# Kernel optimization log

Hardware: AMD Instinct MI355X
Metric: run time of the kernel (lower is better)

Reference implementation:

```python
import jax, jax.numpy as jnp
import numpy as np

WIN = 8          # window size (8x8), hardcoded in SelfAttention
DIM_HEAD = 32    # hardcoded dim_head
LN_EPS = 1e-5


def _rel_pos_index():
    # Reproduces the buffer computed in SelfAttention.__init__ (torch.meshgrid default = 'ij')
    coords = np.stack(np.meshgrid(np.arange(WIN), np.arange(WIN), indexing='ij'))  # (2,8,8)
    flat = coords.reshape(2, -1)                      # (2,64)
    rel = flat[:, :, None] - flat[:, None, :]         # (2,64,64)
    rel = rel.transpose(1, 2, 0).copy()               # (64,64,2)
    rel[:, :, 0] += WIN - 1
    rel[:, :, 1] += WIN - 1
    rel[:, :, 0] *= 2 * WIN - 1
    return jnp.asarray(rel.sum(-1))                   # (64,64) int32, values in [0,225)

REL_IDX = _rel_pos_index()


def setup_inputs() -> dict:
    key = jax.random.key(0)
    ks = jax.random.split(key, 8)
    B, H, W, C = 16, 64, 64, 512
    nh = C // DIM_HEAD
    N = WIN * WIN
    nwin = B * (H // WIN) * (W // WIN)   # 1024 windows total
    inner = 4 * C                        # MLP(expansion_ratio=4, gated=False)
    s = 0.02
    return {
        'x': jax.random.normal(ks[0], (B, H, W, C), jnp.float32),
        'q': jax.random.normal(ks[1], (nwin, N, C), jnp.float32),
        'k': jax.random.normal(ks[2], (nwin, N, C), jnp.float32),
        'v': jax.random.normal(ks[3], (nwin, N, C), jnp.float32),
        'proj_w': jax.random.normal(ks[4], (C, C), jnp.float32) * s,
        'proj_b': jnp.zeros((C,), jnp.float32),
        'rpb_table': jax.random.normal(ks[5], ((2 * WIN - 1) ** 2, nh), jnp.float32) * s,
        'gamma1': jnp.full((C,), 1e-5, jnp.float32),   # LayerScale init_values
        'ln2_w': jnp.ones((C,), jnp.float32),
        'ln2_b': jnp.zeros((C,), jnp.float32),
        'fc1_w': jax.random.normal(ks[6], (inner, C), jnp.float32) * s,
        'fc1_b': jnp.zeros((inner,), jnp.float32),
        'fc2_w': jax.random.normal(ks[7], (C, inner), jnp.float32) * s,
        'fc2_b': jnp.zeros((C,), jnp.float32),
        'gamma2': jnp.full((C,), 1e-5, jnp.float32),
    }


def _layernorm(x, w, b):
    mu = x.mean(-1, keepdims=True)
    var = ((x - mu) ** 2).mean(-1, keepdims=True)
    return (x - mu) * jax.lax.rsqrt(var + LN_EPS) * w + b


def _block(x, q, k, v, proj_w, proj_b, rpb_table, gamma1, ln2_w, ln2_b,
           fc1_w, fc1_b, fc2_w, fc2_b, gamma2):
    B, H, W, C = x.shape
    nh = C // DIM_HEAD
    N = WIN * WIN
    scale = DIM_HEAD ** -0.5
    BW = q.shape[0]  # B * num_windows
    # heads: (BW, nh, N, dh)
    qh = q.reshape(BW, N, nh, DIM_HEAD).transpose(0, 2, 1, 3)
    kh = k.reshape(BW, N, nh, DIM_HEAD).transpose(0, 2, 1, 3)
    vh = v.reshape(BW, N, nh, DIM_HEAD).transpose(0, 2, 1, 3)
    attn = jnp.einsum('bhnd,bhmd->bhnm', qh, kh) * scale
    attn = jax.nn.softmax(attn, axis=-1)
    # NOTE: faithful to source — relative-position bias is added AFTER softmax.
    bias = rpb_table[REL_IDX].transpose(2, 0, 1)  # (nh, 64, 64)
    attn = attn + bias[None]
    out = jnp.einsum('bhnm,bhmd->bhnd', attn, vh)
    out = out.transpose(0, 2, 1, 3).reshape(BW, N, C)
    out = out @ proj_w.T + proj_b
    # window_reverse -> (B, H, W, C)
    attn_out = out.reshape(B, H // WIN, W // WIN, WIN, WIN, C)
    attn_out = attn_out.transpose(0, 1, 3, 2, 4, 5).reshape(B, H, W, C)
    x = x + gamma1 * attn_out                      # LayerScale residual
    h = _layernorm(x, ln2_w, ln2_b)
    h = jax.nn.gelu(h @ fc1_w.T + fc1_b, approximate=False) @ fc2_w.T + fc2_b
    return x + gamma2 * h


def reference(x, q, k, v, proj_w, proj_b, rpb_table, gamma1, ln2_w, ln2_b,
              fc1_w, fc1_b, fc2_w, fc2_b, gamma2):
    return _block(x, q, k, v, proj_w, proj_b, rpb_table, gamma1, ln2_w, ln2_b,
                  fc1_w, fc1_b, fc2_w, fc2_b, gamma2)
```

## Files before the change

kernel.cpp:

```cpp
#include <hip/hip_runtime.h>
#include <math.h>

typedef __attribute__((ext_vector_type(4))) float f32x4;
typedef __attribute__((ext_vector_type(8))) short bf16x8;
typedef __attribute__((ext_vector_type(4))) unsigned short u16x4;
typedef __attribute__((ext_vector_type(8))) unsigned short u16x8;

__device__ __forceinline__ unsigned short f2bf(float f) {
  union { float f; unsigned u; } v; v.f = f;
  return (unsigned short)((v.u + 0x7fffu + ((v.u >> 16) & 1u)) >> 16);
}

__device__ __forceinline__ f32x4 zero4() {
  f32x4 z; z[0] = z[1] = z[2] = z[3] = 0.f; return z;
}

__device__ __forceinline__ f32x4 mfma16(bf16x8 a, bf16x8 b, f32x4 c) {
  return __builtin_amdgcn_mfma_f32_16x16x32_bf16(a, b, c, 0, 0, 0);
}

__device__ __forceinline__ void gload_lds16(const void* g, void* l) {
  __builtin_amdgcn_global_load_lds(
      (const __attribute__((address_space(1))) unsigned int*)g,
      (__attribute__((address_space(3))) unsigned int*)l, 16, 0, 0);
}

__global__ void cvt_kernel(const float* __restrict__ pw, const float* __restrict__ f1,
                           const float* __restrict__ f2, const float* __restrict__ lnw,
                           const float* __restrict__ lnb, const float* __restrict__ f1b,
                           unsigned short* __restrict__ opw, unsigned short* __restrict__ ow1,
                           unsigned short* __restrict__ of2, float* __restrict__ of1bp) {
  const long stride = (long)gridDim.x * blockDim.x;
  const long t0 = (long)blockIdx.x * blockDim.x + threadIdx.x;
  for (long i = t0; i < 512L * 512; i += stride) opw[i] = f2bf(pw[i]);
  for (long i = t0; i < 2048L * 512; i += stride)
    ow1[i] = f2bf(f1[i] * lnw[i & 511]);
  for (long i = t0; i < 512L * 2048; i += stride) of2[i] = f2bf(f2[i]);
  for (long i = t0; i < 2048; i += stride) {
    float s = f1b[i];
    const float* fr = f1 + i * 512;
    for (int c = 0; c < 512; ++c) s += fr[c] * lnb[c];
    of1bp[i] = s;
  }
}

__global__ __launch_bounds__(256) void attn_kernel(
    const float* __restrict__ q, const float* __restrict__ k,
    const float* __restrict__ v, const float* __restrict__ rpb,
    unsigned short* __restrict__ O) {
  __shared__ __align__(16) unsigned short Plds[4][64][72];
  const int w = blockIdx.x;
  const int tid = threadIdx.x;
  const int wv = tid >> 6;
  const int lane = tid & 63;
  const int l16 = lane & 15;
  const int g = lane >> 4;
  unsigned short (*P)[72] = Plds[wv];
  const float scale = 0.17677669529663687f;
  const long base = (long)w * (64 * 512);

  for (int hi = 0; hi < 4; ++hi) {
    const int h = wv * 4 + hi;
    bf16x8 aq[4], bk[4];
#pragma unroll
    for (int t = 0; t < 4; ++t) {
      const float* qp = q + base + (long)(t * 16 + l16) * 512 + h * 32 + g * 8;
      const float* kp = k + base + (long)(t * 16 + l16) * 512 + h * 32 + g * 8;
      f32x4 q0 = *(const f32x4*)qp, q1 = *(const f32x4*)(qp + 4);
      f32x4 k0 = *(const f32x4*)kp, k1 = *(const f32x4*)(kp + 4);
#pragma unroll
      for (int j = 0; j < 4; ++j) {
        aq[t][j]     = (short)f2bf(q0[j] * scale);
        aq[t][j + 4] = (short)f2bf(q1[j] * scale);
        bk[t][j]     = (short)f2bf(k0[j]);
        bk[t][j + 4] = (short)f2bf(k1[j]);
      }
    }
    f32x4 acc[4][4];
#pragma unroll
    for (int a = 0; a < 4; ++a)
#pragma unroll
      for (int b = 0; b < 4; ++b) acc[a][b] = zero4();
#pragma unroll
    for (int a = 0; a < 4; ++a)
#pragma unroll
      for (int b = 0; b < 4; ++b) acc[a][b] = mfma16(aq[a], bk[b], acc[a][b]);

#pragma unroll
    for (int tm = 0; tm < 4; ++tm) {
      f32x4 mx;
#pragma unroll
      for (int i = 0; i < 4; ++i)
        mx[i] = fmaxf(fmaxf(acc[tm][0][i], acc[tm][1][i]),
                      fmaxf(acc[tm][2][i], acc[tm][3][i]));
#pragma unroll
      for (int off = 1; off < 16; off <<= 1)
#pragma unroll
        for (int i = 0; i < 4; ++i)
          mx[i] = fmaxf(mx[i], __shfl_xor(mx[i], off, 64));
      f32x4 sm = zero4();
#pragma unroll
      for (int tc = 0; tc < 4; ++tc)
#pragma unroll
        for (int i = 0; i < 4; ++i) {
          acc[tm][tc][i] = __expf(acc[tm][tc][i] - mx[i]);
          sm[i] += acc[tm][tc][i];
        }
#pragma unroll
      for (int off = 1; off < 16; off <<= 1)
#pragma unroll
        for (int i = 0; i < 4; ++i) sm[i] += __shfl_xor(sm[i], off, 64);
      f32x4 inv;
#pragma unroll
      for (int i = 0; i < 4; ++i) inv[i] = 1.0f / sm[i];
#pragma unroll
      for (int tc = 0; tc < 4; ++tc)
#pragma unroll
        for (int i = 0; i < 4; ++i) {
          int n = tm * 16 + g * 4 + i;
          int m = tc * 16 + l16;
          int idx = ((n >> 3) - (m >> 3) + 7) * 15 + ((n & 7) - (m & 7) + 7);
          P[n][m] = f2bf(acc[tm][tc][i] * inv[i] + rpb[idx * 16 + h]);
        }
    }

    f32x4 oc[4][2];
#pragma unroll
    for (int a = 0; a < 4; ++a) { oc[a][0] = zero4(); oc[a][1] = zero4(); }
#pragma unroll
    for (int ks = 0; ks < 2; ++ks) {
      bf16x8 ap[4];
#pragma unroll
      for (int tm = 0; tm < 4; ++tm)
        ap[tm] = *(const bf16x8*)&P[tm * 16 + l16][ks * 32 + g * 8];
      bf16x8 bv[2];
#pragma unroll
      for (int tn = 0; tn < 2; ++tn)
#pragma unroll
        for (int j = 0; j < 8; ++j) {
          int m = ks * 32 + g * 8 + j;
          bv[tn][j] = (short)f2bf(v[base + (long)m * 512 + h * 32 + tn * 16 + l16]);
        }
#pragma unroll
      for (int tm = 0; tm < 4; ++tm)
#pragma unroll
        for (int tn = 0; tn < 2; ++tn) oc[tm][tn] = mfma16(ap[tm], bv[tn], oc[tm][tn]);
    }
#pragma unroll
    for (int tm = 0; tm < 4; ++tm)
#pragma unroll
      for (int tn = 0; tn < 2; ++tn)
#pragma unroll
        for (int i = 0; i < 4; ++i) {
          int n = tm * 16 + g * 4 + i;
          O[base + (long)n * 512 + h * 32 + tn * 16 + l16] = f2bf(oc[tm][tn][i]);
        }
  }
}

__global__ __launch_bounds__(256) void proj_kernel(
    const unsigned short* __restrict__ O, const unsigned short* __restrict__ pw,
    const float* __restrict__ pb, const float* __restrict__ gamma1,
    const float* __restrict__ x, float* __restrict__ y) {
  const int w = blockIdx.x;
  const int tid = threadIdx.x;
  const int wv = tid >> 6, lane = tid & 63;
  const int l16 = lane & 15, g = lane >> 4;
  const long obase = (long)w * (64 * 512);
  f32x4 acc[4][8];
#pragma unroll
  for (int a = 0; a < 4; ++a)
#pragma unroll
    for (int b = 0; b < 8; ++b) acc[a][b] = zero4();

  for (int kk = 0; kk < 512; kk += 32) {
    bf16x8 a[4];
#pragma unroll
    for (int tm = 0; tm < 4; ++tm)
      a[tm] = *(const bf16x8*)(O + obase + (long)(tm * 16 + l16) * 512 + kk + g * 8);
#pragma unroll
    for (int tn = 0; tn < 8; ++tn) {
      int c = wv * 128 + tn * 16 + l16;
      bf16x8 b = *(const bf16x8*)(pw + (long)c * 512 + kk + g * 8);
#pragma unroll
      for (int tm = 0; tm < 4; ++tm) acc[tm][tn] = mfma16(a[tm], b, acc[tm][tn]);
    }
  }
  const int bi = w >> 6, wh = (w >> 3) & 7, wc = w & 7;
#pragma unroll
  for (int tn = 0; tn < 8; ++tn) {
    int c = wv * 128 + tn * 16 + l16;
    float g1c = gamma1[c], pbc = pb[c];
#pragma unroll
    for (int tm = 0; tm < 4; ++tm)
#pragma unroll
      for (int i = 0; i < 4; ++i) {
        int n = tm * 16 + g * 4 + i;
        long t = (long)(bi * 64 + wh * 8 + (n >> 3)) * 64 + wc * 8 + (n & 7);
        y[t * 512 + c] = x[t * 512 + c] + g1c * (acc[tm][tn][i] + pbc);
      }
  }
}

__global__ __launch_bounds__(256) void ln_stats_kernel(const float* __restrict__ y,
                                                       float* __restrict__ murs) {
  const int tid = threadIdx.x;
  const long row = (long)blockIdx.x * 64 + (tid >> 2);
  const int sg = tid & 3;
  const float* yr = y + row * 512 + sg * 128;
  float s = 0.f, s2 = 0.f;
  for (int j = 0; j < 128; j += 4) {
    f32x4 t = *(const f32x4*)(yr + j);
    s += t[0] + t[1] + t[2] + t[3];
    s2 += t[0] * t[0] + t[1] * t[1] + t[2] * t[2] + t[3] * t[3];
  }
  s += __shfl_xor(s, 1, 64);  s += __shfl_xor(s, 2, 64);
  s2 += __shfl_xor(s2, 1, 64); s2 += __shfl_xor(s2, 2, 64);
  if (sg == 0) {
    float mu = s * (1.f / 512.f);
    murs[row * 2] = mu;
    murs[row * 2 + 1] = rsqrtf(s2 * (1.f / 512.f) - mu * mu + 1e-5f);
  }
}

__global__ __launch_bounds__(256, 3) void fc1_kernel(
    const float* __restrict__ y, const float* __restrict__ murs,
    const unsigned short* __restrict__ w1s, const float* __restrict__ f1bp,
    unsigned short* __restrict__ h1, int tok0) {
  __shared__ __align__(16) unsigned char smem[17408];
  unsigned short* As = (unsigned short*)smem;
  unsigned short* Bs = (unsigned short*)(smem + 8192);
  unsigned short* ep = (unsigned short*)smem;
  const int bid = blockIdx.x;
  const int ct = bid & 15, rt = bid >> 4;
  const int c0 = ct * 128;
  const int tid = threadIdx.x;
  const int wv = tid >> 6, lane = tid & 63;
  const int l16 = lane & 15, g = lane >> 4;
  const int wr = wv >> 1, wc = wv & 1;
  const long t0 = (long)tok0 + (long)rt * 128;

  const int sr = tid >> 1, sh = tid & 1;
  const float mu = murs[(t0 + sr) * 2];
  const float rs = murs[(t0 + sr) * 2 + 1];
  const float* xr = y + (t0 + sr) * 512 + sh * 16;

  f32x4 acc[4][4];
#pragma unroll
  for (int a = 0; a < 4; ++a)
#pragma unroll
    for (int b = 0; b < 4; ++b) acc[a][b] = zero4();

  for (int kk = 0; kk < 512; kk += 32) {
    f32x4 xv[4];
#pragma unroll
    for (int j = 0; j < 4; ++j) xv[j] = *(const f32x4*)(xr + kk + j * 4);
    u16x8 p0, p1;
#pragma unroll
    for (int e = 0; e < 4; ++e) {
      p0[e]     = f2bf((xv[0][e] - mu) * rs);
      p0[e + 4] = f2bf((xv[1][e] - mu) * rs);
      p1[e]     = f2bf((xv[2][e] - mu) * rs);
      p1[e + 4] = f2bf((xv[3][e] - mu) * rs);
    }
    *(u16x8*)(As + sr * 32 + sh * 16) = p0;
    *(u16x8*)(As + sr * 32 + sh * 16 + 8) = p1;
#pragma unroll
    for (int iss = 0; iss < 2; ++iss) {
      int r = wv * 32 + iss * 16 + (lane >> 2);
      gload_lds16(w1s + (long)(c0 + r) * 512 + kk + (lane & 3) * 8,
                  Bs + (wv * 32 + iss * 16) * 32);
    }
    __syncthreads();
    bf16x8 a[4], b[4];
#pragma unroll
    for (int tm = 0; tm < 4; ++tm)
      a[tm] = *(const bf16x8*)(As + (wr * 64 + tm * 16 + l16) * 32 + g * 8);
#pragma unroll
    for (int tn = 0; tn < 4; ++tn)
      b[tn] = *(const bf16x8*)(Bs + (wc * 64 + tn * 16 + l16) * 32 + g * 8);
#pragma unroll
    for (int tm = 0; tm < 4; ++tm)
#pragma unroll
      for (int tn = 0; tn < 4; ++tn) acc[tm][tn] = mfma16(a[tm], b[tn], acc[tm][tn]);
    __syncthreads();
  }

#pragma unroll
  for (int cc = 0; cc < 2; ++cc) {
    if (wc == cc) {
#pragma unroll
      for (int tm = 0; tm < 4; ++tm)
#pragma unroll
        for (int tn = 0; tn < 4; ++tn)
#pragma unroll
          for (int i = 0; i < 4; ++i) {
            int row = wr * 64 + tm * 16 + g * 4 + i;
            int col = tn * 16 + l16;
            float v = acc[tm][tn][i] + f1bp[c0 + cc * 64 + col];
            float ge = 0.5f * v * (1.f + erff(v * 0.70710678118654752f));
            ep[row * 68 + col] = f2bf(ge);
          }
    }
    __syncthreads();
    const int row = tid >> 1, hf = tid & 1;
    unsigned short* dst = h1 + ((long)rt * 128 + row) * 2048 + c0 + cc * 64 + hf * 32;
#pragma unroll
    for (int j = 0; j < 4; ++j)
      *(u16x8*)(dst + j * 8) = *(const u16x8*)(ep + row * 68 + hf * 32 + j * 8);
    __syncthreads();
  }
}

__global__ __launch_bounds__(256, 3) void fc2_kernel(
    const unsigned short* __restrict__ h1, const unsigned short* __restrict__ w2,
    const float* __restrict__ f2b, const float* __restrict__ g2,
    float* __restrict__ y, int tok0) {
  __shared__ __align__(16) unsigned short As[128 * 32];
  __shared__ __align__(16) unsigned short Bs[128 * 32];
  const int bid = blockIdx.x;
  const int ct = bid & 3, rt = bid >> 2;
  const int c0 = ct * 128;
  const int tid = threadIdx.x;
  const int wv = tid >> 6, lane = tid & 63;
  const int l16 = lane & 15, g = lane >> 4;
  const int wr = wv >> 1, wc = wv & 1;

  f32x4 acc[4][4];
#pragma unroll
  for (int a = 0; a < 4; ++a)
#pragma unroll
    for (int b = 0; b < 4; ++b) acc[a][b] = zero4();

  for (int kk = 0; kk < 2048; kk += 32) {
#pragma unroll
    for (int iss = 0; iss < 2; ++iss) {
      int r = wv * 32 + iss * 16 + (lane >> 2);
      int cb = (lane & 3) * 8;
      gload_lds16(h1 + ((long)rt * 128 + r) * 2048 + kk + cb,
                  As + (wv * 32 + iss * 16) * 32);
      gload_lds16(w2 + (long)(c0 + r) * 2048 + kk + cb,
                  Bs + (wv * 32 + iss * 16) * 32);
    }
    __syncthreads();
    bf16x8 a[4], b[4];
#pragma unroll
    for (int tm = 0; tm < 4; ++tm)
      a[tm] = *(const bf16x8*)(As + (wr * 64 + tm * 16 + l16) * 32 + g * 8);
#pragma unroll
    for (int tn = 0; tn < 4; ++tn)
      b[tn] = *(const bf16x8*)(Bs + (wc * 64 + tn * 16 + l16) * 32 + g * 8);
#pragma unroll
    for (int tm = 0; tm < 4; ++tm)
#pragma unroll
      for (int tn = 0; tn < 4; ++tn) acc[tm][tn] = mfma16(a[tm], b[tn], acc[tm][tn]);
    __syncthreads();
  }

#pragma unroll
  for (int tn = 0; tn < 4; ++tn) {
    int c = c0 + wc * 64 + tn * 16 + l16;
    float gc = g2[c], bc = f2b[c];
#pragma unroll
    for (int tm = 0; tm < 4; ++tm)
#pragma unroll
      for (int i = 0; i < 4; ++i) {
        long t = (long)tok0 + (long)rt * 128 + wr * 64 + tm * 16 + g * 4 + i;
        y[t * 512 + c] += gc * (acc[tm][tn][i] + bc);
      }
  }
}

extern "C" void kernel_launch(void* const* d_in, const int* in_sizes, int n_in,
                              void* d_out, int out_size, void* d_ws, size_t ws_size,
                              hipStream_t stream) {
  const float* x   = (const float*)d_in[0];
  const float* q   = (const float*)d_in[1];
  const float* k   = (const float*)d_in[2];
  const float* v   = (const float*)d_in[3];
  const float* pw  = (const float*)d_in[4];
  const float* pb  = (const float*)d_in[5];
  const float* rpb = (const float*)d_in[6];
  const float* g1  = (const float*)d_in[7];
  const float* lnw = (const float*)d_in[8];
  const float* lnb = (const float*)d_in[9];
  const float* f1w = (const float*)d_in[10];
  const float* f1b = (const float*)d_in[11];
  const float* f2w = (const float*)d_in[12];
  const float* f2b = (const float*)d_in[13];
  const float* g2  = (const float*)d_in[14];
  float* y = (float*)d_out;

  unsigned short* Ob   = (unsigned short*)d_ws;
  unsigned short* opw  = Ob + (size_t)1024 * 64 * 512;
  unsigned short* ow1  = opw + 512 * 512;
  unsigned short* of2  = ow1 + 2048 * 512;
  float* of1bp = (float*)(of2 + 512 * 2048);
  float* murs  = of1bp + 2048;
  unsigned short* h1 = Ob;

  hipLaunchKernelGGL(cvt_kernel, dim3(1024), dim3(256), 0, stream,
                     pw, f1w, f2w, lnw, lnb, f1b, opw, ow1, of2, of1bp);
  hipLaunchKernelGGL(attn_kernel, dim3(1024), dim3(256), 0, stream,
                     q, k, v, rpb, Ob);
  hipLaunchKernelGGL(proj_kernel, dim3(1024), dim3(256), 0, stream,
                     Ob, opw, pb, g1, x, y);
  hipLaunchKernelGGL(ln_stats_kernel, dim3(1024), dim3(256), 0, stream, y, murs);
  for (int p = 0; p < 4; ++p) {
    hipLaunchKernelGGL(fc1_kernel, dim3(2048), dim3(256), 0, stream,
                       y, murs, ow1, of1bp, h1, p * 16384);
    hipLaunchKernelGGL(fc2_kernel, dim3(512), dim3(256), 0, stream,
                       h1, of2, f2b, g2, y, p * 16384);
  }
}
```

Measured before the change: 1.442 ms.

## Split attention across head-quad blocks and tile proj GEMM via LDS

The attention kernel now launches one block per (window, group of 4 heads), with each wave handling a single head, so there are four times more blocks and less serial work per block. The relative-position bias slice is staged into shared memory. The projection kernel is restructured into 128x128 output tiles whose A and B operands are loaded into LDS with direct global-to-LDS loads, and the window-reverse address mapping moves into the epilogue. The aim is more parallelism and better operand reuse than the old per-wave direct global loads, at the cost of extra barriers and launch-bound occupancy hints.

```diff
diff --git a/kernel.cpp b/kernel.cpp
--- a/kernel.cpp
+++ b/kernel.cpp
@@ -44,12 +44,14 @@
   }
 }
 
-__global__ __launch_bounds__(256) void attn_kernel(
+__global__ __launch_bounds__(256, 3) void attn_kernel(
     const float* __restrict__ q, const float* __restrict__ k,
     const float* __restrict__ v, const float* __restrict__ rpb,
     unsigned short* __restrict__ O) {
   __shared__ __align__(16) unsigned short Plds[4][64][72];
-  const int w = blockIdx.x;
+  __shared__ float rpb_s[225 * 4];
+  const int w = blockIdx.x >> 2;
+  const int hq = blockIdx.x & 3;
   const int tid = threadIdx.x;
   const int wv = tid >> 6;
   const int lane = tid & 63;
@@ -58,145 +60,165 @@
   unsigned short (*P)[72] = Plds[wv];
   const float scale = 0.17677669529663687f;
   const long base = (long)w * (64 * 512);
-
-  for (int hi = 0; hi < 4; ++hi) {
-    const int h = wv * 4 + hi;
-    bf16x8 aq[4], bk[4];
-#pragma unroll
-    for (int t = 0; t < 4; ++t) {
-      const float* qp = q + base + (long)(t * 16 + l16) * 512 + h * 32 + g * 8;
-      const float* kp = k + base + (long)(t * 16 + l16) * 512 + h * 32 + g * 8;
-      f32x4 q0 = *(const f32x4*)qp, q1 = *(const f32x4*)(qp + 4);
-      f32x4 k0 = *(const f32x4*)kp, k1 = *(const f32x4*)(kp + 4);
-#pragma unroll
-      for (int j = 0; j < 4; ++j) {
-        aq[t][j]     = (short)f2bf(q0[j] * scale);
-        aq[t][j + 4] = (short)f2bf(q1[j] * scale);
-        bk[t][j]     = (short)f2bf(k0[j]);
-        bk[t][j + 4] = (short)f2bf(k1[j]);
-      }
-    }
-    f32x4 acc[4][4];
-#pragma unroll
-    for (int a = 0; a < 4; ++a)
-#pragma unroll
-      for (int b = 0; b < 4; ++b) acc[a][b] = zero4();
-#pragma unroll
-    for (int a = 0; a < 4; ++a)
-#pragma unroll
-      for (int b = 0; b < 4; ++b) acc[a][b] = mfma16(aq[a], bk[b], acc[a][b]);
-
-#pragma unroll
-    for (int tm = 0; tm < 4; ++tm) {
-      f32x4 mx;
+  const int h = hq * 4 + wv;
+
+  for (int i = tid; i < 225 * 4; i += 256)
+    rpb_s[i] = rpb[(i >> 2) * 16 + hq * 4 + (i & 3)];
+  __syncthreads();
+
+  bf16x8 aq[4], bk[4];
+#pragma unroll
+  for (int t = 0; t < 4; ++t) {
+    const float* qp = q + base + (long)(t * 16 + l16) * 512 + h * 32 + g * 8;
+    const float* kp = k + base + (long)(t * 16 + l16) * 512 + h * 32 + g * 8;
+    f32x4 q0 = *(const f32x4*)qp, q1 = *(const f32x4*)(qp + 4);
+    f32x4 k0 = *(const f32x4*)kp, k1 = *(const f32x4*)(kp + 4);
+#pragma unroll
+    for (int j = 0; j < 4; ++j) {
+      aq[t][j]     = (short)f2bf(q0[j] * scale);
+      aq[t][j + 4] = (short)f2bf(q1[j] * scale);
+      bk[t][j]     = (short)f2bf(k0[j]);
+      bk[t][j + 4] = (short)f2bf(k1[j]);
+    }
+  }
+  f32x4 acc[4][4];
+#pragma unroll
+  for (int a = 0; a < 4; ++a)
+#pragma unroll
+    for (int b = 0; b < 4; ++b) acc[a][b] = zero4();
+#pragma unroll
+  for (int a = 0; a < 4; ++a)
+#pragma unroll
+    for (int b = 0; b < 4; ++b) acc[a][b] = mfma16(aq[a], bk[b], acc[a][b]);
+
+#pragma unroll
+  for (int tm = 0; tm < 4; ++tm) {
+    f32x4 mx;
+#pragma unroll
+    for (int i = 0; i < 4; ++i)
+      mx[i] = fmaxf(fmaxf(acc[tm][0][i], acc[tm][1][i]),
+                    fmaxf(acc[tm][2][i], acc[tm][3][i]));
+#pragma unroll
+    for (int off = 1; off < 16; off <<= 1)
 #pragma unroll
       for (int i = 0; i < 4; ++i)
-        mx[i] = fmaxf(fmaxf(acc[tm][0][i], acc[tm][1][i]),
-                      fmaxf(acc[tm][2][i], acc[tm][3][i]));
-#pragma unroll
-      for (int off = 1; off < 16; off <<= 1)
-#pragma unroll
-        for (int i = 0; i < 4; ++i)
-          mx[i] = fmaxf(mx[i], __shfl_xor(mx[i], off, 64));
-      f32x4 sm = zero4();
-#pragma unroll
-      for (int tc = 0; tc < 4; ++tc)
-#pragma unroll
-        for (int i = 0; i < 4; ++i) {
-          acc[tm][tc][i] = __expf(acc[tm][tc][i] - mx[i]);
-          sm[i] += acc[tm][tc][i];
-        }
-#pragma unroll
-      for (int off = 1; off < 16; off <<= 1)
-#pragma unroll
-        for (int i = 0; i < 4; ++i) sm[i] += __shfl_xor(sm[i], off, 64);
-      f32x4 inv;
-#pragma unroll
-      for (int i = 0; i < 4; ++i) inv[i] = 1.0f / sm[i];
-#pragma unroll
-      for (int tc = 0; tc < 4; ++tc)
-#pragma unroll
-        for (int i = 0; i < 4; ++i) {
-          int n = tm * 16 + g * 4 + i;
-          int m = tc * 16 + l16;
-          int idx = ((n >> 3) - (m >> 3) + 7) * 15 + ((n & 7) - (m & 7) + 7);
-          P[n][m] = f2bf(acc[tm][tc][i] * inv[i] + rpb[idx * 16 + h]);
-        }
-    }
-
-    f32x4 oc[4][2];
-#pragma unroll
-    for (int a = 0; a < 4; ++a) { oc[a][0] = zero4(); oc[a][1] = zero4(); }
-#pragma unroll
-    for (int ks = 0; ks < 2; ++ks) {
-      bf16x8 ap[4];
-#pragma unroll
-      for (int tm = 0; tm < 4; ++tm)
-        ap[tm] = *(const bf16x8*)&P[tm * 16 + l16][ks * 32 + g * 8];
-      bf16x8 bv[2];
-#pragma unroll
-      for (int tn = 0; tn < 2; ++tn)
-#pragma unroll
-        for (int j = 0; j < 8; ++j) {
-          int m = ks * 32 + g * 8 + j;
-          bv[tn][j] = (short)f2bf(v[base + (long)m * 512 + h * 32 + tn * 16 + l16]);
-        }
-#pragma unroll
-      for (int tm = 0; tm < 4; ++tm)
-#pragma unroll
-        for (int tn = 0; tn < 2; ++tn) oc[tm][tn] = mfma16(ap[tm], bv[tn], oc[tm][tn]);
-    }
-#pragma unroll
-    for (int tm = 0; tm < 4; ++tm)
-#pragma unroll
-      for (int tn = 0; tn < 2; ++tn)
-#pragma unroll
-        for (int i = 0; i < 4; ++i) {
-          int n = tm * 16 + g * 4 + i;
-          O[base + (long)n * 512 + h * 32 + tn * 16 + l16] = f2bf(oc[tm][tn][i]);
-        }
-  }
-}
-
-__global__ __launch_bounds__(256) void proj_kernel(
+        mx[i] = fmaxf(mx[i], __shfl_xor(mx[i], off, 64));
+    f32x4 sm = zero4();
+#pragma unroll
+    for (int tc = 0; tc < 4; ++tc)
+#pragma unroll
+      for (int i = 0; i < 4; ++i) {
+        acc[tm][tc][i] = __expf(acc[tm][tc][i] - mx[i]);
+        sm[i] += acc[tm][tc][i];
+      }
+#pragma unroll
+    for (int off = 1; off < 16; off <<= 1)
+#pragma unroll
+      for (int i = 0; i < 4; ++i) sm[i] += __shfl_xor(sm[i], off, 64);
+    f32x4 inv;
+#pragma unroll
+    for (int i = 0; i < 4; ++i) inv[i] = 1.0f / sm[i];
+#pragma unroll
+    for (int tc = 0; tc < 4; ++tc)
+#pragma unroll
+      for (int i = 0; i < 4; ++i) {
+        int n = tm * 16 + g * 4 + i;
+        int m = tc * 16 + l16;
+        int idx = ((n >> 3) - (m >> 3) + 7) * 15 + ((n & 7) - (m & 7) + 7);
+        P[n][m] = f2bf(acc[tm][tc][i] * inv[i] + rpb_s[idx * 4 + wv]);
+      }
+  }
+
+  f32x4 oc[4][2];
+#pragma unroll
+  for (int a = 0; a < 4; ++a) { oc[a][0] = zero4(); oc[a][1] = zero4(); }
+#pragma unroll
+  for (int ks = 0; ks < 2; ++ks) {
+    bf16x8 ap[4];
+#pragma unroll
+    for (int tm = 0; tm < 4; ++tm)
+      ap[tm] = *(const bf16x8*)&P[tm * 16 + l16][ks * 32 + g * 8];
+    bf16x8 bv[2];
+#pragma unroll
+    for (int tn = 0; tn < 2; ++tn)
+#pragma unroll
+      for (int j = 0; j < 8; ++j) {
+        int m = ks * 32 + g * 8 + j;
+        bv[tn][j] = (short)f2bf(v[base + (long)m * 512 + h * 32 + tn * 16 + l16]);
+      }
+#pragma unroll
+    for (int tm = 0; tm < 4; ++tm)
+#pragma unroll
+      for (int tn = 0; tn < 2; ++tn) oc[tm][tn] = mfma16(ap[tm], bv[tn], oc[tm][tn]);
+  }
+#pragma unroll
+  for (int tm = 0; tm < 4; ++tm)
+#pragma unroll
+    for (int tn = 0; tn < 2; ++tn)
+#pragma unroll
+      for (int i = 0; i < 4; ++i) {
+        int n = tm * 16 + g * 4 + i;
+        O[base + (long)n * 512 + h * 32 + tn * 16 + l16] = f2bf(oc[tm][tn][i]);
+      }
+}
+
+__global__ __launch_bounds__(256, 3) void proj_kernel(
     const unsigned short* __restrict__ O, const unsigned short* __restrict__ pw,
     const float* __restrict__ pb, const float* __restrict__ gamma1,
     const float* __restrict__ x, float* __restrict__ y) {
-  const int w = blockIdx.x;
+  __shared__ __align__(16) unsigned short As[128 * 32];
+  __shared__ __align__(16) unsigned short Bs[128 * 32];
+  const int bid = blockIdx.x;
+  const int ct = bid & 3, rt = bid >> 2;
+  const int c0 = ct * 128;
   const int tid = threadIdx.x;
   const int wv = tid >> 6, lane = tid & 63;
   const int l16 = lane & 15, g = lane >> 4;
-  const long obase = (long)w * (64 * 512);
-  f32x4 acc[4][8];
+  const int wr = wv >> 1, wc = wv & 1;
+
+  f32x4 acc[4][4];
 #pragma unroll
   for (int a = 0; a < 4; ++a)
 #pragma unroll
-    for (int b = 0; b < 8; ++b) acc[a][b] = zero4();
+    for (int b = 0; b < 4; ++b) acc[a][b] = zero4();
 
   for (int kk = 0; kk < 512; kk += 32) {
-    bf16x8 a[4];
-#pragma unroll
-    for (int tm = 0; tm < 4; ++tm)
-      a[tm] = *(const bf16x8*)(O + obase + (long)(tm * 16 + l16) * 512 + kk + g * 8);
-#pragma unroll
-    for (int tn = 0; tn < 8; ++tn) {
-      int c = wv * 128 + tn * 16 + l16;
-      bf16x8 b = *(const bf16x8*)(pw + (long)c * 512 + kk + g * 8);
-#pragma unroll
-      for (int tm = 0; tm < 4; ++tm) acc[tm][tn] = mfma16(a[tm], b, acc[tm][tn]);
-    }
-  }
-  const int bi = w >> 6, wh = (w >> 3) & 7, wc = w & 7;
-#pragma unroll
-  for (int tn = 0; tn < 8; ++tn) {
-    int c = wv * 128 + tn * 16 + l16;
+#pragma unroll
+    for (int iss = 0; iss < 2; ++iss) {
+      int r = wv * 32 + iss * 16 + (lane >> 2);
+      int cb = (lane & 3) * 8;
+      gload_lds16(O + ((long)rt * 128 + r) * 512 + kk + cb,
+                  As + (wv * 32 + iss * 16) * 32);
+      gload_lds16(pw + (long)(c0 + r) * 512 + kk + cb,
+                  Bs + (wv * 32 + iss * 16) * 32);
+    }
+    __syncthreads();
+    bf16x8 a[4], b[4];
+#pragma unroll
+    for (int tm = 0; tm < 4; ++tm)
+      a[tm] = *(const bf16x8*)(As + (wr * 64 + tm * 16 + l16) * 32 + g * 8);
+#pragma unroll
+    for (int tn = 0; tn < 4; ++tn)
+      b[tn] = *(const bf16x8*)(Bs + (wc * 64 + tn * 16 + l16) * 32 + g * 8);
+#pragma unroll
+    for (int tm = 0; tm < 4; ++tm)
+#pragma unroll
+      for (int tn = 0; tn < 4; ++tn) acc[tm][tn] = mfma16(a[tm], b[tn], acc[tm][tn]);
+    __syncthreads();
+  }
+
+#pragma unroll
+  for (int tn = 0; tn < 4; ++tn) {
+    int c = c0 + wc * 64 + tn * 16 + l16;
     float g1c = gamma1[c], pbc = pb[c];
 #pragma unroll
     for (int tm = 0; tm < 4; ++tm)
 #pragma unroll
       for (int i = 0; i < 4; ++i) {
-        int n = tm * 16 + g * 4 + i;
-        long t = (long)(bi * 64 + wh * 8 + (n >> 3)) * 64 + wc * 8 + (n & 7);
+        int t2 = rt * 128 + wr * 64 + tm * 16 + g * 4 + i;
+        int ww = t2 >> 6, n = t2 & 63;
+        int bi = ww >> 6, wh = (ww >> 3) & 7, wcol = ww & 7;
+        long t = (long)(bi * 64 + wh * 8 + (n >> 3)) * 64 + wcol * 8 + (n & 7);
         y[t * 512 + c] = x[t * 512 + c] + g1c * (acc[tm][tn][i] + pbc);
       }
   }
@@ -401,9 +423,9 @@
 
   hipLaunchKernelGGL(cvt_kernel, dim3(1024), dim3(256), 0, stream,
                      pw, f1w, f2w, lnw, lnb, f1b, opw, ow1, of2, of1bp);
-  hipLaunchKernelGGL(attn_kernel, dim3(1024), dim3(256), 0, stream,
+  hipLaunchKernelGGL(attn_kernel, dim3(4096), dim3(256), 0, stream,
                      q, k, v, rpb, Ob);
-  hipLaunchKernelGGL(proj_kernel, dim3(1024), dim3(256), 0, stream,
+  hipLaunchKernelGGL(proj_kernel, dim3(2048), dim3(256), 0, stream,
                      Ob, opw, pb, g1, x, y);
   hipLaunchKernelGGL(ln_stats_kernel, dim3(1024), dim3(256), 0, stream, y, murs);
   for (int p = 0; p < 4; ++p) {
```

After: 1.305 ms. 9.5% less time.
